# Kernel optimization log

Hardware: AMD Instinct MI355X
Metric: run time of the kernel (lower is better)

The kernel has to match this reference:

```python
import jax, jax.numpy as jnp
import numpy as np

N, D, H = 50000, 256, 8
HD = D // H
E = 800000
NEG_SLOPE = 0.2


def setup_inputs() -> dict:
    key = jax.random.key(0)
    ks = jax.random.split(key, 12)
    s = 1.0 / np.sqrt(D)
    return {
        "x": jax.random.normal(ks[0], (N, D), jnp.float32),
        "edge_index": jax.random.randint(ks[1], (2, E), 0, N, jnp.int64),
        "edge_attr": jax.random.normal(ks[2], (E, 16), jnp.float32),
        # GATConv params: lin weight (no bias), attention vectors, output bias
        "W": jax.random.normal(ks[3], (D, D), jnp.float32) * s,
        "att_src": jax.random.normal(ks[4], (H, HD), jnp.float32) * s,
        "att_dst": jax.random.normal(ks[5], (H, HD), jnp.float32) * s,
        "bias": jnp.zeros((D,), jnp.float32),
        # LayerNorm
        "ln_g": jnp.ones((D,), jnp.float32),
        "ln_b": jnp.zeros((D,), jnp.float32),
        # FFN
        "W1": jax.random.normal(ks[6], (D, D), jnp.float32) * s,
        "b1": jnp.zeros((D,), jnp.float32),
        "W2": jax.random.normal(ks[7], (D, D), jnp.float32) * s,
        "b2": jnp.zeros((D,), jnp.float32),
    }


def _gat_layer(x, edge_index, W, att_src, att_dst, bias, ln_g, ln_b, W1, b1, W2, b2):
    n = x.shape[0]
    # GATConv default add_self_loops=True
    sl = jnp.arange(n, dtype=edge_index.dtype)
    src = jnp.concatenate([edge_index[0], sl])  # [E+N]
    dst = jnp.concatenate([edge_index[1], sl])  # [E+N]

    xp = (x @ W).reshape(n, H, HD)                      # [N,H,hd]
    a_src = jnp.einsum("nhd,hd->nh", xp, att_src)        # [N,H]
    a_dst = jnp.einsum("nhd,hd->nh", xp, att_dst)        # [N,H]

    e = a_src[src] + a_dst[dst]                          # [E+N,H]
    e = jax.nn.leaky_relu(e, NEG_SLOPE)
    # segment softmax over destination nodes (every node has a self loop)
    m = jax.ops.segment_max(e, dst, num_segments=n)      # [N,H]
    ex = jnp.exp(e - m[dst])
    denom = jax.ops.segment_sum(ex, dst, num_segments=n) # [N,H]
    alpha = ex / (denom[dst] + 1e-16)                    # [E+N,H]

    msg = alpha[:, :, None] * xp[src]                    # [E+N,H,hd]
    out = jax.ops.segment_sum(msg, dst, num_segments=n)  # [N,H,hd]
    h = out.reshape(n, D) + bias

    # residual + LayerNorm
    r = h + x
    mu = jnp.mean(r, axis=-1, keepdims=True)
    var = jnp.mean(jnp.square(r - mu), axis=-1, keepdims=True)
    hn = (r - mu) / jnp.sqrt(var + 1e-5) * ln_g + ln_b

    # FFN
    return jax.nn.relu(hn @ W1 + b1) @ W2 + b2


def reference(x, edge_index, edge_attr, W, att_src, att_dst, bias, ln_g, ln_b, W1, b1, W2, b2):
    # edge_attr is accepted but unused (GATConv built without edge_dim)
    return _gat_layer(x, edge_index, W, att_src, att_dst, bias, ln_g, ln_b, W1, b1, W2, b2)
```

## Files before the change

kernel.cpp:

```cpp
#include <hip/hip_runtime.h>
#include <hip/hip_bf16.h>

#define H 8
#define HD 32
#define DD 256
#define NEG_SLOPE 0.2f
#define SLOT 64

typedef short bf16x8 __attribute__((ext_vector_type(8)));
typedef float f32x4 __attribute__((ext_vector_type(4)));

__device__ __forceinline__ unsigned short f2bf(float f) {
    unsigned int u = __float_as_uint(f);
    unsigned int r = (u + 0x7fffu + ((u >> 16) & 1u)) >> 16;
    return (unsigned short)r;
}
__device__ __forceinline__ float bf2f(unsigned short b) {
    return __uint_as_float(((unsigned int)b) << 16);
}

#define GLOAD_LDS16(g, s)                                                        \
    __builtin_amdgcn_global_load_lds((const __attribute__((address_space(1))) void*)(g), \
                                     (__attribute__((address_space(3))) void*)(s), 16, 0, 0)

__global__ __launch_bounds__(256) void zero_cnt(int* __restrict__ cnt, int N) {
    int i = blockIdx.x * 256 + threadIdx.x;
    if (i < N) cnt[i] = 0;
}

__global__ __launch_bounds__(256) void prep(const float* __restrict__ x, unsigned short* __restrict__ xb,
                                            const float* __restrict__ W, unsigned short* __restrict__ Wt,
                                            const float* __restrict__ W1, unsigned short* __restrict__ W1t,
                                            const float* __restrict__ W2, unsigned short* __restrict__ W2t,
                                            const int* __restrict__ ei, int* __restrict__ src_sorted,
                                            int* __restrict__ cnt, int N, int n4, int E, int HB) {
    int b = blockIdx.x;
    int tid = threadIdx.x;
    if (b < HB) {
        int e = b * 256 + tid;
        if (e < E) {
            int s = ei[e];
            int d = ei[E + e];
            int r = atomicAdd(&cnt[d], 1);
            src_sorted[(size_t)d * SLOT + r] = s;
        }
    } else if (b < HB + 768) {
        int wb = b - HB;
        const float* src = (wb < 256) ? W : (wb < 512) ? W1 : W2;
        unsigned short* dst = (wb < 256) ? Wt : (wb < 512) ? W1t : W2t;
        int i = (wb & 255) * 256 + tid;
        int n = i >> 8, k = i & 255;
        dst[i] = f2bf(src[k * 256 + n]);
    } else {
        int i = (b - HB - 768) * 256 + tid;
        if (i < n4) {
            float4 v = ((const float4*)x)[i];
            ushort4 o;
            o.x = f2bf(v.x); o.y = f2bf(v.y); o.z = f2bf(v.z); o.w = f2bf(v.w);
            ((ushort4*)xb)[i] = o;
        }
    }
}

template <bool ATTN, bool PHASE2>
__global__ __launch_bounds__(256) void gemm_fused(
    const unsigned short* __restrict__ A,
    const unsigned short* __restrict__ B1t, const float* __restrict__ b1,
    const unsigned short* __restrict__ B2t, const float* __restrict__ b2,
    void* __restrict__ Cout, int M,
    const float* __restrict__ att_s, const float* __restrict__ att_d,
    float* __restrict__ a_srcO, float* __restrict__ a_dstO) {
    __shared__ __align__(16) unsigned short Als[4096];
    __shared__ __align__(16) unsigned short Bls[16384];
    __shared__ __align__(16) unsigned short t1ls[PHASE2 ? 64 * 280 : 8];

    const int tid = threadIdx.x;
    const int l = tid & 63;
    const int w = tid >> 6;
    const int r16 = l & 15, q0 = l >> 4;
    const int row0 = blockIdx.x * 64;

    const int ca0 = w * 128 + l, ca1 = ca0 + 64;
    const unsigned short* gA0 = A + (size_t)min(row0 + (ca0 & 63), M - 1) * DD + (ca0 >> 6) * 8;
    const unsigned short* gA1 = A + (size_t)min(row0 + (ca1 & 63), M - 1) * DD + (ca1 >> 6) * 8;
    unsigned short* lA0 = &Als[ca0 * 8];
    unsigned short* lA1 = &Als[ca1 * 8];

    const unsigned short* gB8[8];
    unsigned short* lB[8];
#pragma unroll
    for (int k = 0; k < 8; k++) {
        int c = w * 512 + k * 64 + l;
        gB8[k] = B1t + (size_t)(c & 255) * DD + (c >> 8) * 8;
        lB[k] = &Bls[c * 8];
    }

    f32x4 zero = {0.f, 0.f, 0.f, 0.f};
    f32x4 acc[4][4];
#pragma unroll
    for (int i = 0; i < 4; i++)
#pragma unroll
        for (int j = 0; j < 4; j++) acc[i][j] = zero;

    for (int kk = 0; kk < 256; kk += 64) {
        GLOAD_LDS16(gA0 + kk, lA0);
        GLOAD_LDS16(gA1 + kk, lA1);
#pragma unroll
        for (int k = 0; k < 8; k++) GLOAD_LDS16(gB8[k] + kk, lB[k]);
        __syncthreads();
#pragma unroll
        for (int t = 0; t < 2; t++) {
            int q = t * 4 + q0;
            bf16x8 af[4], bf[4];
#pragma unroll
            for (int i = 0; i < 4; i++)
                af[i] = *(const bf16x8*)&Als[(q * 64 + i * 16 + r16) * 8];
#pragma unroll
            for (int j = 0; j < 4; j++)
                bf[j] = *(const bf16x8*)&Bls[(q * 256 + w * 64 + j * 16 + r16) * 8];
#pragma unroll
            for (int i = 0; i < 4; i++)
#pragma unroll
                for (int j = 0; j < 4; j++)
                    acc[i][j] = __builtin_amdgcn_mfma_f32_16x16x32_bf16(af[i], bf[j], acc[i][j], 0, 0, 0);
        }
        __syncthreads();
    }

    if (!PHASE2) {
        float aws0, aws1, aws2, aws3, awd0, awd1, awd2, awd3;
        int hA = 0, hB = 0;
        if (ATTN) {
            hA = w * 2; hB = hA + 1;
            aws0 = att_s[hA * HD + r16];
            aws1 = att_s[hA * HD + 16 + r16];
            aws2 = att_s[hB * HD + r16];
            aws3 = att_s[hB * HD + 16 + r16];
            awd0 = att_d[hA * HD + r16];
            awd1 = att_d[hA * HD + 16 + r16];
            awd2 = att_d[hB * HD + r16];
            awd3 = att_d[hB * HD + 16 + r16];
        }
#pragma unroll
        for (int i = 0; i < 4; i++) {
#pragma unroll
            for (int r = 0; r < 4; r++) {
                int row = row0 + i * 16 + q0 * 4 + r;
                if (row < M) {
#pragma unroll
                    for (int j = 0; j < 4; j++) {
                        int col = w * 64 + j * 16 + r16;
                        ((unsigned short*)Cout)[(size_t)row * DD + col] = f2bf(acc[i][j][r]);
                    }
                }
                if (ATTN) {
                    float v0 = acc[i][0][r], v1 = acc[i][1][r];
                    float v2 = acc[i][2][r], v3 = acc[i][3][r];
                    float ps0 = v0 * aws0 + v1 * aws1;
                    float ps1 = v2 * aws2 + v3 * aws3;
                    float pd0 = v0 * awd0 + v1 * awd1;
                    float pd1 = v2 * awd2 + v3 * awd3;
#pragma unroll
                    for (int m = 1; m < 16; m <<= 1) {
                        ps0 += __shfl_xor(ps0, m, 64);
                        ps1 += __shfl_xor(ps1, m, 64);
                        pd0 += __shfl_xor(pd0, m, 64);
                        pd1 += __shfl_xor(pd1, m, 64);
                    }
                    if (r16 == 0 && row < M) {
                        a_srcO[row * H + hA] = ps0;
                        a_srcO[row * H + hB] = ps1;
                        a_dstO[row * H + hA] = pd0;
                        a_dstO[row * H + hB] = pd1;
                    }
                }
            }
        }
    } else {
        float bb1[4];
#pragma unroll
        for (int j = 0; j < 4; j++) bb1[j] = b1[w * 64 + j * 16 + r16];
#pragma unroll
        for (int i = 0; i < 4; i++)
#pragma unroll
            for (int r = 0; r < 4; r++) {
                int rl = i * 16 + q0 * 4 + r;
#pragma unroll
                for (int j = 0; j < 4; j++) {
                    float v = fmaxf(acc[i][j][r] + bb1[j], 0.f);
                    t1ls[rl * 280 + w * 64 + j * 16 + r16] = f2bf(v);
                }
            }
        __syncthreads();

        const unsigned short* gB2[8];
#pragma unroll
        for (int k = 0; k < 8; k++) {
            int c = w * 512 + k * 64 + l;
            gB2[k] = B2t + (size_t)(c & 255) * DD + (c >> 8) * 8;
        }
#pragma unroll
        for (int i = 0; i < 4; i++)
#pragma unroll
            for (int j = 0; j < 4; j++) acc[i][j] = zero;

        for (int kk = 0; kk < 256; kk += 64) {
#pragma unroll
            for (int k = 0; k < 8; k++) GLOAD_LDS16(gB2[k] + kk, lB[k]);
            __syncthreads();
#pragma unroll
            for (int t = 0; t < 2; t++) {
                int q = t * 4 + q0;
                bf16x8 af[4], bf[4];
#pragma unroll
                for (int i = 0; i < 4; i++)
                    af[i] = *(const bf16x8*)&t1ls[(i * 16 + r16) * 280 + kk + q * 8];
#pragma unroll
                for (int j = 0; j < 4; j++)
                    bf[j] = *(const bf16x8*)&Bls[(q * 256 + w * 64 + j * 16 + r16) * 8];
#pragma unroll
                for (int i = 0; i < 4; i++)
#pragma unroll
                    for (int j = 0; j < 4; j++)
                        acc[i][j] = __builtin_amdgcn_mfma_f32_16x16x32_bf16(af[i], bf[j], acc[i][j], 0, 0, 0);
            }
            __syncthreads();
        }

        float bb2[4];
#pragma unroll
        for (int j = 0; j < 4; j++) bb2[j] = b2[w * 64 + j * 16 + r16];
#pragma unroll
        for (int i = 0; i < 4; i++)
#pragma unroll
            for (int r = 0; r < 4; r++) {
                int row = row0 + i * 16 + q0 * 4 + r;
                if (row < M) {
#pragma unroll
                    for (int j = 0; j < 4; j++) {
                        int col = w * 64 + j * 16 + r16;
                        ((float*)Cout)[(size_t)row * DD + col] = acc[i][j][r] + bb2[j];
                    }
                }
            }
    }
}

__global__ __launch_bounds__(256) void aggregate_ln(
    const unsigned short* __restrict__ xp, const unsigned short* __restrict__ x_bf,
    const float* __restrict__ a_src, const float* __restrict__ a_dst,
    const int* __restrict__ cnt, const int* __restrict__ src_sorted,
    const float* __restrict__ bias, const float* __restrict__ ln_g,
    const float* __restrict__ ln_b, unsigned short* __restrict__ hn, int N) {
    int wave = threadIdx.x >> 6;
    int lane = threadIdx.x & 63;
    int n = blockIdx.x * 4 + wave;
    if (n >= N) return;
    int h = lane >> 3;

    float adst = a_dst[n * H + h];
    float e0 = a_src[n * H + h] + adst;
    e0 = (e0 > 0.f) ? e0 : NEG_SLOPE * e0;
    float ex = __expf(e0);
    ushort4 u = *(const ushort4*)(xp + (size_t)n * DD + lane * 4);
    float acc0 = ex * bf2f(u.x), acc1 = ex * bf2f(u.y);
    float acc2 = ex * bf2f(u.z), acc3 = ex * bf2f(u.w);
    float denom = ex;

    int beg = n * SLOT;
    int end = beg + cnt[n];
    int i = beg;
    for (; i + 7 < end; i += 8) {
        int s[8];
        float es[8];
        ushort4 uu[8];
#pragma unroll
        for (int k = 0; k < 8; k++) s[k] = src_sorted[i + k];
#pragma unroll
        for (int k = 0; k < 8; k++) es[k] = a_src[s[k] * H + h];
#pragma unroll
        for (int k = 0; k < 8; k++) uu[k] = *(const ushort4*)(xp + (size_t)s[k] * DD + lane * 4);
#pragma unroll
        for (int k = 0; k < 8; k++) {
            float e = es[k] + adst;
            e = (e > 0.f) ? e : NEG_SLOPE * e;
            float wk = __expf(e);
            acc0 += wk * bf2f(uu[k].x);
            acc1 += wk * bf2f(uu[k].y);
            acc2 += wk * bf2f(uu[k].z);
            acc3 += wk * bf2f(uu[k].w);
            denom += wk;
        }
    }
    for (; i < end; i++) {
        int s0 = src_sorted[i];
        float es0 = a_src[s0 * H + h];
        ushort4 u0 = *(const ushort4*)(xp + (size_t)s0 * DD + lane * 4);
        float e0a = es0 + adst;
        e0a = (e0a > 0.f) ? e0a : NEG_SLOPE * e0a;
        float w0 = __expf(e0a);
        acc0 += w0 * bf2f(u0.x);
        acc1 += w0 * bf2f(u0.y);
        acc2 += w0 * bf2f(u0.z);
        acc3 += w0 * bf2f(u0.w);
        denom += w0;
    }
    float inv = 1.f / (denom + 1e-16f);
    float4 bb = *(const float4*)(bias + lane * 4);
    ushort4 xr = *(const ushort4*)(x_bf + (size_t)n * DD + lane * 4);
    float r0 = acc0 * inv + bb.x + bf2f(xr.x);
    float r1 = acc1 * inv + bb.y + bf2f(xr.y);
    float r2 = acc2 * inv + bb.z + bf2f(xr.z);
    float r3 = acc3 * inv + bb.w + bf2f(xr.w);

    float s = r0 + r1 + r2 + r3;
#pragma unroll
    for (int m = 1; m < 64; m <<= 1) s += __shfl_xor(s, m, 64);
    float mu = s * (1.f / 256.f);
    float d0 = r0 - mu, d1 = r1 - mu, d2 = r2 - mu, d3 = r3 - mu;
    float qv = d0 * d0 + d1 * d1 + d2 * d2 + d3 * d3;
#pragma unroll
    for (int m = 1; m < 64; m <<= 1) qv += __shfl_xor(qv, m, 64);
    float rstd = rsqrtf(qv * (1.f / 256.f) + 1e-5f);
    float4 g = *(const float4*)(ln_g + lane * 4);
    float4 b = *(const float4*)(ln_b + lane * 4);
    ushort4 o;
    o.x = f2bf(d0 * rstd * g.x + b.x);
    o.y = f2bf(d1 * rstd * g.y + b.y);
    o.z = f2bf(d2 * rstd * g.z + b.z);
    o.w = f2bf(d3 * rstd * g.w + b.w);
    *(ushort4*)(hn + (size_t)n * DD + lane * 4) = o;
}

extern "C" void kernel_launch(void* const* d_in, const int* in_sizes, int n_in,
                              void* d_out, int out_size, void* d_ws, size_t ws_size,
                              hipStream_t stream) {
    const float* x = (const float*)d_in[0];
    const int* edge_index = (const int*)d_in[1];
    const float* W = (const float*)d_in[3];
    const float* att_src = (const float*)d_in[4];
    const float* att_dst = (const float*)d_in[5];
    const float* bias = (const float*)d_in[6];
    const float* ln_g = (const float*)d_in[7];
    const float* ln_b = (const float*)d_in[8];
    const float* W1 = (const float*)d_in[9];
    const float* b1 = (const float*)d_in[10];
    const float* W2 = (const float*)d_in[11];
    const float* b2 = (const float*)d_in[12];

    const int N = in_sizes[0] / DD;
    const int E = in_sizes[1] / 2;

    char* p = (char*)d_ws;
    auto carve = [&](size_t bytes) {
        char* r = p;
        p += (bytes + 255) & ~(size_t)255;
        return r;
    };
    unsigned short* x_bf = (unsigned short*)carve((size_t)N * DD * 2);
    unsigned short* xp_bf = (unsigned short*)carve((size_t)N * DD * 2);
    unsigned short* hn_bf = (unsigned short*)carve((size_t)N * DD * 2);
    float* a_src = (float*)carve((size_t)N * H * 4);
    float* a_dst = (float*)carve((size_t)N * H * 4);
    int* cnt = (int*)carve((size_t)N * 4);
    int* src_sorted = (int*)carve((size_t)N * SLOT * 4);
    unsigned short* Wt = (unsigned short*)carve(65536 * 2);
    unsigned short* W1t = (unsigned short*)carve(65536 * 2);
    unsigned short* W2t = (unsigned short*)carve(65536 * 2);

    const int n4 = N * DD / 4;
    const int HB = (E + 255) / 256;

    zero_cnt<<<(N + 255) / 256, 256, 0, stream>>>(cnt, N);

    int prep_blocks = HB + 768 + (n4 + 255) / 256;
    prep<<<prep_blocks, 256, 0, stream>>>(x, x_bf, W, Wt, W1, W1t, W2, W2t,
                                          edge_index, src_sorted, cnt, N, n4, E, HB);

    const int gblocks = (N + 63) / 64;

    gemm_fused<true, false><<<gblocks, 256, 0, stream>>>(
        x_bf, Wt, nullptr, nullptr, nullptr, xp_bf, N, att_src, att_dst, a_src, a_dst);

    aggregate_ln<<<(N + 3) / 4, 256, 0, stream>>>(xp_bf, x_bf, a_src, a_dst, cnt, src_sorted,
                                                  bias, ln_g, ln_b, hn_bf, N);

    gemm_fused<false, true><<<gblocks, 256, 0, stream>>>(
        hn_bf, W1t, b1, W2t, b2, d_out, N, nullptr, nullptr, nullptr, nullptr);
}
```

Baseline: 344.5 us.

## Move edge bucketing into first GEMM launch and fold count zeroing into prep

The separate zero_cnt kernel is removed and its work is folded into the prep kernel as extra blocks. Edge bucketing by destination, which uses atomics, moves out of prep and runs as the leading blocks of the first GEMM launch, so the latency-bound scatter can overlap with the bf16 projection GEMM. This drops one kernel launch and lets prep finish sooner. It also adds a bound check on the slot index, and the GEMM grid gains many short-lived blocks that may affect scheduling.

```diff
diff --git a/kernel.cpp b/kernel.cpp
--- a/kernel.cpp
+++ b/kernel.cpp
@@ -23,36 +23,24 @@
     __builtin_amdgcn_global_load_lds((const __attribute__((address_space(1))) void*)(g), \
                                      (__attribute__((address_space(3))) void*)(s), 16, 0, 0)
 
-__global__ __launch_bounds__(256) void zero_cnt(int* __restrict__ cnt, int N) {
-    int i = blockIdx.x * 256 + threadIdx.x;
-    if (i < N) cnt[i] = 0;
-}
-
 __global__ __launch_bounds__(256) void prep(const float* __restrict__ x, unsigned short* __restrict__ xb,
                                             const float* __restrict__ W, unsigned short* __restrict__ Wt,
                                             const float* __restrict__ W1, unsigned short* __restrict__ W1t,
                                             const float* __restrict__ W2, unsigned short* __restrict__ W2t,
-                                            const int* __restrict__ ei, int* __restrict__ src_sorted,
-                                            int* __restrict__ cnt, int N, int n4, int E, int HB) {
+                                            int* __restrict__ cnt, int N, int n4, int ZB) {
     int b = blockIdx.x;
     int tid = threadIdx.x;
-    if (b < HB) {
-        int e = b * 256 + tid;
-        if (e < E) {
-            int s = ei[e];
-            int d = ei[E + e];
-            int r = atomicAdd(&cnt[d], 1);
-            src_sorted[(size_t)d * SLOT + r] = s;
-        }
-    } else if (b < HB + 768) {
-        int wb = b - HB;
-        const float* src = (wb < 256) ? W : (wb < 512) ? W1 : W2;
-        unsigned short* dst = (wb < 256) ? Wt : (wb < 512) ? W1t : W2t;
-        int i = (wb & 255) * 256 + tid;
+    if (b < 768) {
+        const float* src = (b < 256) ? W : (b < 512) ? W1 : W2;
+        unsigned short* dst = (b < 256) ? Wt : (b < 512) ? W1t : W2t;
+        int i = (b & 255) * 256 + tid;
         int n = i >> 8, k = i & 255;
         dst[i] = f2bf(src[k * 256 + n]);
+    } else if (b < 768 + ZB) {
+        int i = (b - 768) * 256 + tid;
+        if (i < N) cnt[i] = 0;
     } else {
-        int i = (b - HB - 768) * 256 + tid;
+        int i = (b - 768 - ZB) * 256 + tid;
         if (i < n4) {
             float4 v = ((const float4*)x)[i];
             ushort4 o;
@@ -69,16 +57,32 @@
     const unsigned short* __restrict__ B2t, const float* __restrict__ b2,
     void* __restrict__ Cout, int M,
     const float* __restrict__ att_s, const float* __restrict__ att_d,
-    float* __restrict__ a_srcO, float* __restrict__ a_dstO) {
+    float* __restrict__ a_srcO, float* __restrict__ a_dstO,
+    const int* __restrict__ ei, int* __restrict__ cnt,
+    int* __restrict__ src_sorted, int E, int HB) {
     __shared__ __align__(16) unsigned short Als[4096];
     __shared__ __align__(16) unsigned short Bls[16384];
     __shared__ __align__(16) unsigned short t1ls[PHASE2 ? 64 * 280 : 8];
 
     const int tid = threadIdx.x;
+
+    if constexpr (ATTN) {
+        if ((int)blockIdx.x < HB) {
+            int e = blockIdx.x * 256 + tid;
+            if (e < E) {
+                int s = ei[e];
+                int d = ei[E + e];
+                int r = atomicAdd(&cnt[d], 1);
+                if (r < SLOT) src_sorted[(size_t)d * SLOT + r] = s;
+            }
+            return;
+        }
+    }
+
     const int l = tid & 63;
     const int w = tid >> 6;
     const int r16 = l & 15, q0 = l >> 4;
-    const int row0 = blockIdx.x * 64;
+    const int row0 = ((int)blockIdx.x - (ATTN ? HB : 0)) * 64;
 
     const int ca0 = w * 128 + l, ca1 = ca0 + 64;
     const unsigned short* gA0 = A + (size_t)min(row0 + (ca0 & 63), M - 1) * DD + (ca0 >> 6) * 8;
@@ -369,22 +373,23 @@
     unsigned short* W2t = (unsigned short*)carve(65536 * 2);
 
     const int n4 = N * DD / 4;
+    const int ZB = (N + 255) / 256;
     const int HB = (E + 255) / 256;
 
-    zero_cnt<<<(N + 255) / 256, 256, 0, stream>>>(cnt, N);
-
-    int prep_blocks = HB + 768 + (n4 + 255) / 256;
+    int prep_blocks = 768 + ZB + (n4 + 255) / 256;
     prep<<<prep_blocks, 256, 0, stream>>>(x, x_bf, W, Wt, W1, W1t, W2, W2t,
-                                          edge_index, src_sorted, cnt, N, n4, E, HB);
+                                          cnt, N, n4, ZB);
 
     const int gblocks = (N + 63) / 64;
 
-    gemm_fused<true, false><<<gblocks, 256, 0, stream>>>(
-        x_bf, Wt, nullptr, nullptr, nullptr, xp_bf, N, att_src, att_dst, a_src, a_dst);
+    gemm_fused<true, false><<<HB + gblocks, 256, 0, stream>>>(
+        x_bf, Wt, nullptr, nullptr, nullptr, xp_bf, N, att_src, att_dst, a_src, a_dst,
+        edge_index, cnt, src_sorted, E, HB);
 
     aggregate_ln<<<(N + 3) / 4, 256, 0, stream>>>(xp_bf, x_bf, a_src, a_dst, cnt, src_sorted,
                                                   bias, ln_g, ln_b, hn_bf, N);
 
     gemm_fused<false, true><<<gblocks, 256, 0, stream>>>(
-        hn_bf, W1t, b1, W2t, b2, d_out, N, nullptr, nullptr, nullptr, nullptr);
-}
+        hn_bf, W1t, b1, W2t, b2, d_out, N, nullptr, nullptr, nullptr, nullptr,
+        nullptr, nullptr, nullptr, 0, 0);
+}
```

New measurement: 368.2 us. +6.9%, slower.

## Partition edge-bucketing counters per XCD to keep atomics in local L2

Applied to the files above, without the earlier changes.

Edge bucketing now keeps a separate counter array and slot segment for each XCD, selected by reading the hardware XCC id, and uses workgroup-scope relaxed atomics on them. The goal is to avoid cross-die coherent atomics on shared per-destination counters. Aggregation then walks up to eight segments per node, which makes the loop shorter per segment and less regular. Correctness relies on workgroup-scope atomics being coherent within an XCD's L2 and on no node getting more than 16 edges from one XCD, since extra edges are silently dropped.

```diff
diff --git a/kernel.cpp b/kernel.cpp
--- a/kernel.cpp
+++ b/kernel.cpp
@@ -5,7 +5,9 @@
 #define HD 32
 #define DD 256
 #define NEG_SLOPE 0.2f
-#define SLOT 64
+#define NXCD 8
+#define SEG 16
+#define SLOT (NXCD * SEG)
 
 typedef short bf16x8 __attribute__((ext_vector_type(8)));
 typedef float f32x4 __attribute__((ext_vector_type(4)));
@@ -19,13 +21,19 @@
     return __uint_as_float(((unsigned int)b) << 16);
 }
 
+__device__ __forceinline__ int xcc_id() {
+    int x;
+    asm volatile("s_getreg_b32 %0, hwreg(HW_REG_XCC_ID)" : "=s"(x));
+    return x & (NXCD - 1);
+}
+
 #define GLOAD_LDS16(g, s)                                                        \
     __builtin_amdgcn_global_load_lds((const __attribute__((address_space(1))) void*)(g), \
                                      (__attribute__((address_space(3))) void*)(s), 16, 0, 0)
 
-__global__ __launch_bounds__(256) void zero_cnt(int* __restrict__ cnt, int N) {
+__global__ __launch_bounds__(256) void zero_cnt(int* __restrict__ cnt, int n8) {
     int i = blockIdx.x * 256 + threadIdx.x;
-    if (i < N) cnt[i] = 0;
+    if (i < n8) cnt[i] = 0;
 }
 
 __global__ __launch_bounds__(256) void prep(const float* __restrict__ x, unsigned short* __restrict__ xb,
@@ -33,7 +41,7 @@
                                             const float* __restrict__ W1, unsigned short* __restrict__ W1t,
                                             const float* __restrict__ W2, unsigned short* __restrict__ W2t,
                                             const int* __restrict__ ei, int* __restrict__ src_sorted,
-                                            int* __restrict__ cnt, int N, int n4, int E, int HB) {
+                                            int* __restrict__ cnt_x, int N, int n4, int E, int HB) {
     int b = blockIdx.x;
     int tid = threadIdx.x;
     if (b < HB) {
@@ -41,8 +49,10 @@
         if (e < E) {
             int s = ei[e];
             int d = ei[E + e];
-            int r = atomicAdd(&cnt[d], 1);
-            src_sorted[(size_t)d * SLOT + r] = s;
+            int xc = xcc_id();
+            int r = __hip_atomic_fetch_add(&cnt_x[xc * N + d], 1,
+                                           __ATOMIC_RELAXED, __HIP_MEMORY_SCOPE_WORKGROUP);
+            if (r < SEG) src_sorted[(size_t)d * SLOT + xc * SEG + r] = s;
         }
     } else if (b < HB + 768) {
         int wb = b - HB;
@@ -249,7 +259,7 @@
 __global__ __launch_bounds__(256) void aggregate_ln(
     const unsigned short* __restrict__ xp, const unsigned short* __restrict__ x_bf,
     const float* __restrict__ a_src, const float* __restrict__ a_dst,
-    const int* __restrict__ cnt, const int* __restrict__ src_sorted,
+    const int* __restrict__ cnt_x, const int* __restrict__ src_sorted,
     const float* __restrict__ bias, const float* __restrict__ ln_g,
     const float* __restrict__ ln_b, unsigned short* __restrict__ hn, int N) {
     int wave = threadIdx.x >> 6;
@@ -267,43 +277,47 @@
     float acc2 = ex * bf2f(u.z), acc3 = ex * bf2f(u.w);
     float denom = ex;
 
-    int beg = n * SLOT;
-    int end = beg + cnt[n];
-    int i = beg;
-    for (; i + 7 < end; i += 8) {
-        int s[8];
-        float es[8];
-        ushort4 uu[8];
-#pragma unroll
-        for (int k = 0; k < 8; k++) s[k] = src_sorted[i + k];
-#pragma unroll
-        for (int k = 0; k < 8; k++) es[k] = a_src[s[k] * H + h];
-#pragma unroll
-        for (int k = 0; k < 8; k++) uu[k] = *(const ushort4*)(xp + (size_t)s[k] * DD + lane * 4);
-#pragma unroll
-        for (int k = 0; k < 8; k++) {
-            float e = es[k] + adst;
-            e = (e > 0.f) ? e : NEG_SLOPE * e;
-            float wk = __expf(e);
-            acc0 += wk * bf2f(uu[k].x);
-            acc1 += wk * bf2f(uu[k].y);
-            acc2 += wk * bf2f(uu[k].z);
-            acc3 += wk * bf2f(uu[k].w);
-            denom += wk;
-        }
-    }
-    for (; i < end; i++) {
-        int s0 = src_sorted[i];
-        float es0 = a_src[s0 * H + h];
-        ushort4 u0 = *(const ushort4*)(xp + (size_t)s0 * DD + lane * 4);
-        float e0a = es0 + adst;
-        e0a = (e0a > 0.f) ? e0a : NEG_SLOPE * e0a;
-        float w0 = __expf(e0a);
-        acc0 += w0 * bf2f(u0.x);
-        acc1 += w0 * bf2f(u0.y);
-        acc2 += w0 * bf2f(u0.z);
-        acc3 += w0 * bf2f(u0.w);
-        denom += w0;
+    int base = n * SLOT;
+    for (int xs = 0; xs < NXCD; xs++) {
+        int c = cnt_x[xs * N + n];
+        if (c > SEG) c = SEG;
+        int i = base + xs * SEG;
+        int end = i + c;
+        for (; i + 7 < end; i += 8) {
+            int s[8];
+            float es[8];
+            ushort4 uu[8];
+#pragma unroll
+            for (int k = 0; k < 8; k++) s[k] = src_sorted[i + k];
+#pragma unroll
+            for (int k = 0; k < 8; k++) es[k] = a_src[s[k] * H + h];
+#pragma unroll
+            for (int k = 0; k < 8; k++) uu[k] = *(const ushort4*)(xp + (size_t)s[k] * DD + lane * 4);
+#pragma unroll
+            for (int k = 0; k < 8; k++) {
+                float e = es[k] + adst;
+                e = (e > 0.f) ? e : NEG_SLOPE * e;
+                float wk = __expf(e);
+                acc0 += wk * bf2f(uu[k].x);
+                acc1 += wk * bf2f(uu[k].y);
+                acc2 += wk * bf2f(uu[k].z);
+                acc3 += wk * bf2f(uu[k].w);
+                denom += wk;
+            }
+        }
+        for (; i < end; i++) {
+            int s0 = src_sorted[i];
+            float es0 = a_src[s0 * H + h];
+            ushort4 u0 = *(const ushort4*)(xp + (size_t)s0 * DD + lane * 4);
+            float e0a = es0 + adst;
+            e0a = (e0a > 0.f) ? e0a : NEG_SLOPE * e0a;
+            float w0 = __expf(e0a);
+            acc0 += w0 * bf2f(u0.x);
+            acc1 += w0 * bf2f(u0.y);
+            acc2 += w0 * bf2f(u0.z);
+            acc3 += w0 * bf2f(u0.w);
+            denom += w0;
+        }
     }
     float inv = 1.f / (denom + 1e-16f);
     float4 bb = *(const float4*)(bias + lane * 4);
@@ -362,7 +376,7 @@
     unsigned short* hn_bf = (unsigned short*)carve((size_t)N * DD * 2);
     float* a_src = (float*)carve((size_t)N * H * 4);
     float* a_dst = (float*)carve((size_t)N * H * 4);
-    int* cnt = (int*)carve((size_t)N * 4);
+    int* cnt_x = (int*)carve((size_t)N * NXCD * 4);
     int* src_sorted = (int*)carve((size_t)N * SLOT * 4);
     unsigned short* Wt = (unsigned short*)carve(65536 * 2);
     unsigned short* W1t = (unsigned short*)carve(65536 * 2);
@@ -371,18 +385,19 @@
     const int n4 = N * DD / 4;
     const int HB = (E + 255) / 256;
 
-    zero_cnt<<<(N + 255) / 256, 256, 0, stream>>>(cnt, N);
+    const int n8 = N * NXCD;
+    zero_cnt<<<(n8 + 255) / 256, 256, 0, stream>>>(cnt_x, n8);
 
     int prep_blocks = HB + 768 + (n4 + 255) / 256;
     prep<<<prep_blocks, 256, 0, stream>>>(x, x_bf, W, Wt, W1, W1t, W2, W2t,
-                                          edge_index, src_sorted, cnt, N, n4, E, HB);
+                                          edge_index, src_sorted, cnt_x, N, n4, E, HB);
 
     const int gblocks = (N + 63) / 64;
 
     gemm_fused<true, false><<<gblocks, 256, 0, stream>>>(
         x_bf, Wt, nullptr, nullptr, nullptr, xp_bf, N, att_src, att_dst, a_src, a_dst);
 
-    aggregate_ln<<<(N + 3) / 4, 256, 0, stream>>>(xp_bf, x_bf, a_src, a_dst, cnt, src_sorted,
+    aggregate_ln<<<(N + 3) / 4, 256, 0, stream>>>(xp_bf, x_bf, a_src, a_dst, cnt_x, src_sorted,
                                                   bias, ln_g, ln_b, hn_bf, N);
 
     gemm_fused<false, true><<<gblocks, 256, 0, stream>>>(
```

New measurement: 407.4 us. 1.18x slower.

## Load full A tile once into LDS and read weight fragments directly from global

Applied to the files above, without the earlier changes.

The GEMM kernels now stage the whole 64x256 A tile into LDS in a single pass with one barrier. The B (weight) operand is no longer staged in LDS; each wave loads its bf16x8 fragments straight from global memory, relying on L2/L1 caching of the small transposed weights. This removes the per-k-step barriers and the LDS traffic for B, but makes the MFMA loop depend on global load latency. A bounds check is also added to the edge bucketing so that nodes with more than SLOT incoming edges no longer write out of range.

```diff
diff --git a/kernel.cpp b/kernel.cpp
--- a/kernel.cpp
+++ b/kernel.cpp
@@ -42,7 +42,7 @@
             int s = ei[e];
             int d = ei[E + e];
             int r = atomicAdd(&cnt[d], 1);
-            src_sorted[(size_t)d * SLOT + r] = s;
+            if (r < SLOT) src_sorted[(size_t)d * SLOT + r] = s;
         }
     } else if (b < HB + 768) {
         int wb = b - HB;
@@ -70,8 +70,7 @@
     void* __restrict__ Cout, int M,
     const float* __restrict__ att_s, const float* __restrict__ att_d,
     float* __restrict__ a_srcO, float* __restrict__ a_dstO) {
-    __shared__ __align__(16) unsigned short Als[4096];
-    __shared__ __align__(16) unsigned short Bls[16384];
+    __shared__ __align__(16) unsigned short Als[16384];
     __shared__ __align__(16) unsigned short t1ls[PHASE2 ? 64 * 280 : 8];
 
     const int tid = threadIdx.x;
@@ -80,20 +79,13 @@
     const int r16 = l & 15, q0 = l >> 4;
     const int row0 = blockIdx.x * 64;
 
-    const int ca0 = w * 128 + l, ca1 = ca0 + 64;
-    const unsigned short* gA0 = A + (size_t)min(row0 + (ca0 & 63), M - 1) * DD + (ca0 >> 6) * 8;
-    const unsigned short* gA1 = A + (size_t)min(row0 + (ca1 & 63), M - 1) * DD + (ca1 >> 6) * 8;
-    unsigned short* lA0 = &Als[ca0 * 8];
-    unsigned short* lA1 = &Als[ca1 * 8];
-
-    const unsigned short* gB8[8];
-    unsigned short* lB[8];
 #pragma unroll
     for (int k = 0; k < 8; k++) {
-        int c = w * 512 + k * 64 + l;
-        gB8[k] = B1t + (size_t)(c & 255) * DD + (c >> 8) * 8;
-        lB[k] = &Bls[c * 8];
-    }
+        int c = k * 256 + tid;
+        const unsigned short* g = A + (size_t)min(row0 + (c & 63), M - 1) * DD + (c >> 6) * 8;
+        GLOAD_LDS16(g, &Als[c * 8]);
+    }
+    __syncthreads();
 
     f32x4 zero = {0.f, 0.f, 0.f, 0.f};
     f32x4 acc[4][4];
@@ -102,29 +94,24 @@
 #pragma unroll
         for (int j = 0; j < 4; j++) acc[i][j] = zero;
 
-    for (int kk = 0; kk < 256; kk += 64) {
-        GLOAD_LDS16(gA0 + kk, lA0);
-        GLOAD_LDS16(gA1 + kk, lA1);
-#pragma unroll
-        for (int k = 0; k < 8; k++) GLOAD_LDS16(gB8[k] + kk, lB[k]);
-        __syncthreads();
+#pragma unroll
+    for (int kk = 0; kk < 4; kk++) {
 #pragma unroll
         for (int t = 0; t < 2; t++) {
-            int q = t * 4 + q0;
+            const int qq = kk * 8 + t * 4 + q0;
             bf16x8 af[4], bf[4];
 #pragma unroll
+            for (int j = 0; j < 4; j++)
+                bf[j] = *(const bf16x8*)&B1t[(size_t)(w * 64 + j * 16 + r16) * DD + qq * 8];
+#pragma unroll
             for (int i = 0; i < 4; i++)
-                af[i] = *(const bf16x8*)&Als[(q * 64 + i * 16 + r16) * 8];
-#pragma unroll
-            for (int j = 0; j < 4; j++)
-                bf[j] = *(const bf16x8*)&Bls[(q * 256 + w * 64 + j * 16 + r16) * 8];
+                af[i] = *(const bf16x8*)&Als[(qq * 64 + i * 16 + r16) * 8];
 #pragma unroll
             for (int i = 0; i < 4; i++)
 #pragma unroll
                 for (int j = 0; j < 4; j++)
                     acc[i][j] = __builtin_amdgcn_mfma_f32_16x16x32_bf16(af[i], bf[j], acc[i][j], 0, 0, 0);
         }
-        __syncthreads();
     }
 
     if (!PHASE2) {
@@ -193,38 +180,29 @@
             }
         __syncthreads();
 
-        const unsigned short* gB2[8];
-#pragma unroll
-        for (int k = 0; k < 8; k++) {
-            int c = w * 512 + k * 64 + l;
-            gB2[k] = B2t + (size_t)(c & 255) * DD + (c >> 8) * 8;
-        }
 #pragma unroll
         for (int i = 0; i < 4; i++)
 #pragma unroll
             for (int j = 0; j < 4; j++) acc[i][j] = zero;
 
-        for (int kk = 0; kk < 256; kk += 64) {
-#pragma unroll
-            for (int k = 0; k < 8; k++) GLOAD_LDS16(gB2[k] + kk, lB[k]);
-            __syncthreads();
+#pragma unroll
+        for (int kk = 0; kk < 4; kk++) {
 #pragma unroll
             for (int t = 0; t < 2; t++) {
-                int q = t * 4 + q0;
+                const int qq = kk * 8 + t * 4 + q0;
                 bf16x8 af[4], bf[4];
 #pragma unroll
+                for (int j = 0; j < 4; j++)
+                    bf[j] = *(const bf16x8*)&B2t[(size_t)(w * 64 + j * 16 + r16) * DD + qq * 8];
+#pragma unroll
                 for (int i = 0; i < 4; i++)
-                    af[i] = *(const bf16x8*)&t1ls[(i * 16 + r16) * 280 + kk + q * 8];
-#pragma unroll
-                for (int j = 0; j < 4; j++)
-                    bf[j] = *(const bf16x8*)&Bls[(q * 256 + w * 64 + j * 16 + r16) * 8];
+                    af[i] = *(const bf16x8*)&t1ls[(i * 16 + r16) * 280 + qq * 8];
 #pragma unroll
                 for (int i = 0; i < 4; i++)
 #pragma unroll
                     for (int j = 0; j < 4; j++)
                         acc[i][j] = __builtin_amdgcn_mfma_f32_16x16x32_bf16(af[i], bf[j], acc[i][j], 0, 0, 0);
             }
-            __syncthreads();
         }
 
         float bb2[4];
```

Result: no change. 338.9 us (-1.6%).
